# Kernel tuning notes

Hardware: AMD Instinct MI355X
Metric: run time of the kernel (lower is better)

## Reference

```python
import jax, jax.numpy as jnp
import numpy as np

MAX_POINTS = 2048  # config['object_points']


def setup_inputs() -> dict:
    key = jax.random.key(0)
    k1, k2 = jax.random.split(key)
    B, N, C = 64, 131072, 4
    point_cloud = jax.random.normal(k1, (B, N, C), dtype=jnp.float32)
    logits = jax.random.normal(k2, (B, 2, N), dtype=jnp.float32)
    return {"point_cloud": point_cloud, "logits": logits}


def reference(point_cloud, logits):
    """JAX translation of point_cloud_masking.

    point_cloud: (B, N, C) with xyz in channels 0:3
    logits:      (B, 2, N)
    Returns (object_point_cloud (B, M, 3), mask_xyz_mean (B, 3)).
    """
    M = MAX_POINTS
    B, N, _ = point_cloud.shape
    dtype = point_cloud.dtype

    mask = logits[:, 0, :] < logits[:, 1, :]                  # (B, N) bool
    maskf = mask.astype(dtype)
    count_f = jnp.sum(maskf, axis=1)                          # (B,)
    xyz = point_cloud[..., :3]                                # (B, N, 3)
    mask_xyz_mean = jnp.sum(maskf[..., None] * xyz, axis=1) / jnp.maximum(count_f, 1.0)[:, None]  # (B,3)
    centered = xyz - mask_xyz_mean[:, None, :]                # (B, N, 3)

    # Stable argsort puts masked-point indices first, preserving order (like torch.where).
    order = jnp.argsort(1 - maskf, axis=1, stable=True)       # (B, N) int
    cnt = count_f.astype(jnp.int32)                           # (B,)

    # Resample to fixed M points (with replacement), matching torch.randint semantics:
    #   cnt >  M: all M indices random in [0, cnt)
    #   cnt <  M: first cnt identity, remaining random in [0, cnt)
    #   cnt == M: identity
    ksel = jax.random.key(42)
    rand = jax.random.randint(ksel, (B, M), 0, jnp.maximum(cnt, 1)[:, None])
    j = jnp.arange(M, dtype=jnp.int32)[None, :]               # (1, M)
    keep = (j < cnt[:, None]) & (cnt[:, None] <= M)
    sel = jnp.where(keep, j, rand)                            # (B, M) positions into sorted order
    idx = jnp.take_along_axis(order, sel, axis=1)             # (B, M) original point indices
    obj = jnp.take_along_axis(centered, idx[..., None], axis=1)  # (B, M, 3)

    # Empty-mask fallback: ones * batch_index (matches torch branch).
    empty = (cnt == 0)[:, None, None]
    batch_ids = jnp.arange(B, dtype=dtype)[:, None, None]
    obj = jnp.where(empty, jnp.ones_like(obj) * batch_ids, obj)
    return obj, mask_xyz_mean
```

## Files before the change

### kernel.cpp

```cpp
#include <hip/hip_runtime.h>
#include <stdint.h>

#define BATCH 64
#define NPTS  131072
#define MPTS  2048
#define WORDS_PB (NPTS / 64)
#define P1_PPB 4096
#define P1_BLOCKS (BATCH * NPTS / P1_PPB)

struct U2 { uint32_t a, b; };

__host__ __device__ constexpr U2 tf2x32(uint32_t k0, uint32_t k1, uint32_t x0, uint32_t x1) {
  uint32_t ks0 = k0, ks1 = k1, ks2 = k0 ^ k1 ^ 0x1BD11BDAu;
  x0 += ks0; x1 += ks1;
  const int rotA[4] = {13, 15, 26, 6};
  const int rotB[4] = {17, 29, 16, 24};
  for (int r = 0; r < 4; ++r) { x0 += x1; x1 = (x1 << rotA[r]) | (x1 >> (32 - rotA[r])); x1 ^= x0; }
  x0 += ks1; x1 += ks2 + 1u;
  for (int r = 0; r < 4; ++r) { x0 += x1; x1 = (x1 << rotB[r]) | (x1 >> (32 - rotB[r])); x1 ^= x0; }
  x0 += ks2; x1 += ks0 + 2u;
  for (int r = 0; r < 4; ++r) { x0 += x1; x1 = (x1 << rotA[r]) | (x1 >> (32 - rotA[r])); x1 ^= x0; }
  x0 += ks0; x1 += ks1 + 3u;
  for (int r = 0; r < 4; ++r) { x0 += x1; x1 = (x1 << rotB[r]) | (x1 >> (32 - rotB[r])); x1 ^= x0; }
  x0 += ks1; x1 += ks2 + 4u;
  for (int r = 0; r < 4; ++r) { x0 += x1; x1 = (x1 << rotA[r]) | (x1 >> (32 - rotA[r])); x1 ^= x0; }
  x0 += ks2; x1 += ks0 + 5u;
  return U2{x0, x1};
}

__global__ __launch_bounds__(256) void pass1_kernel(
    const float4* __restrict__ pc, const float* __restrict__ lg,
    float* __restrict__ sums, unsigned long long* __restrict__ maskWords) {
  int blk = blockIdx.x;
  int t = threadIdx.x;
  size_t pbase = (size_t)blk * P1_PPB;
  int b = (int)(pbase >> 17);
  const float* l0g = lg + (size_t)b * NPTS;
  const float* l1g = lg + (size_t)(b + 1) * NPTS;

  float sx = 0.f, sy = 0.f, sz = 0.f;
#pragma unroll 2
  for (int half = 0; half < 2; ++half) {
#pragma unroll
    for (int k = 0; k < 8; ++k) {
      size_t p = pbase + (size_t)(half * 8 + k) * 256 + t;
      float a0 = l0g[p];
      float a1 = l1g[p];
      float4 q = pc[p];
      bool m = a0 < a1;
      unsigned long long bal = __ballot(m);
      if ((t & 63) == 0) maskWords[p >> 6] = bal;
      if (m) { sx += q.x; sy += q.y; sz += q.z; }
    }
  }

  for (int o = 32; o; o >>= 1) {
    sx += __shfl_down(sx, o, 64);
    sy += __shfl_down(sy, o, 64);
    sz += __shfl_down(sz, o, 64);
  }
  __shared__ float ssx[4], ssy[4], ssz[4];
  int wave = t >> 6;
  if ((t & 63) == 0) { ssx[wave] = sx; ssy[wave] = sy; ssz[wave] = sz; }
  __syncthreads();
  if (t == 0) {
    atomicAdd(&sums[b * 3 + 0], ssx[0] + ssx[1] + ssx[2] + ssx[3]);
    atomicAdd(&sums[b * 3 + 1], ssy[0] + ssy[1] + ssy[2] + ssy[3]);
    atomicAdd(&sums[b * 3 + 2], ssz[0] + ssz[1] + ssz[2] + ssz[3]);
  }
}

__global__ __launch_bounds__(256) void pass2_kernel(
    const unsigned long long* __restrict__ maskWords, const float* __restrict__ sums,
    uint32_t* __restrict__ wordOff, int* __restrict__ cnt,
    float* __restrict__ mean, float* __restrict__ out) {
  int b = blockIdx.x, t = threadIdx.x;
  int lane = t & 63, wv = t >> 6;
  const unsigned long long* mw = maskWords + (size_t)b * WORDS_PB;
  int base = t * 8;
  int p[8];
  int local = 0;
#pragma unroll
  for (int k = 0; k < 8; ++k) { p[k] = __popcll(mw[base + k]); local += p[k]; }

  int x = local;
#pragma unroll
  for (int o = 1; o < 64; o <<= 1) {
    int y = __shfl_up(x, o, 64);
    if (lane >= o) x += y;
  }
  __shared__ int wsum[4];
  if (lane == 63) wsum[wv] = x;
  __syncthreads();
  int add = 0;
#pragma unroll
  for (int u = 0; u < 4; ++u) add += (u < wv) ? wsum[u] : 0;
  int run = add + x - local;
  uint32_t* wo = wordOff + (size_t)b * WORDS_PB;
#pragma unroll
  for (int k = 0; k < 8; ++k) { wo[base + k] = (uint32_t)run; run += p[k]; }

  if (t == 0) {
    int ct = wsum[0] + wsum[1] + wsum[2] + wsum[3];
    cnt[b] = ct;
    float d  = fmaxf((float)ct, 1.0f);
    float mx = sums[b * 3 + 0] / d;
    float my = sums[b * 3 + 1] / d;
    float mz = sums[b * 3 + 2] / d;
    mean[b * 3 + 0] = mx; mean[b * 3 + 1] = my; mean[b * 3 + 2] = mz;
    float* om = out + (size_t)BATCH * MPTS * 3 + (size_t)b * 3;
    om[0] = mx; om[1] = my; om[2] = mz;
  }
}

__global__ __launch_bounds__(256) void pass3_kernel(
    const float4* __restrict__ pc, const int* __restrict__ cnt,
    const float* __restrict__ mean, const uint32_t* __restrict__ wordOff,
    const unsigned long long* __restrict__ maskWords,
    float* __restrict__ out) {
  int blk = blockIdx.x;
  int b = blk >> 3;
  int t = threadIdx.x;
  int j = (blk & 7) * 256 + t;
  int gid = b * MPTS + j;

  __shared__ uint32_t sOff[WORDS_PB];
  __shared__ float sMean[3];
  __shared__ int sCnt;
  const uint32_t* wo = wordOff + (size_t)b * WORDS_PB;
#pragma unroll
  for (int k = 0; k < 8; ++k) sOff[t + k * 256] = wo[t + k * 256];
  if (t < 3)  sMean[t] = mean[b * 3 + t];
  if (t == 0) sCnt = cnt[b];
  __syncthreads();

  int cb = sCnt;
  float ox, oy, oz;
  if (cb == 0) {
    ox = oy = oz = (float)b;
  } else {
    constexpr U2 K1 = tf2x32(0u, 42u, 0u, 0u);
    constexpr U2 K2 = tf2x32(0u, 42u, 0u, 1u);
    uint32_t span = (uint32_t)cb;
    U2 h = tf2x32(K1.a, K1.b, 0u, (uint32_t)gid);
    U2 l = tf2x32(K2.a, K2.b, 0u, (uint32_t)gid);
    uint32_t hb = h.a ^ h.b;
    uint32_t lb = l.a ^ l.b;
    uint32_t mul = 65536u % span;
    mul = (mul * mul) % span;
    uint32_t off = ((hb % span) * mul + (lb % span)) % span;
    int r = (j < cb && cb <= MPTS) ? j : (int)off;

    int lo = 0;
#pragma unroll
    for (int step = 1024; step; step >>= 1) {
      int nxt = lo + step;
      if (nxt < WORDS_PB && sOff[nxt] <= (uint32_t)r) lo = nxt;
    }
    int rem = r - (int)sOff[lo];
    unsigned long long w = maskWords[(size_t)b * WORDS_PB + lo];

    uint32_t cur = (uint32_t)w;
    int bitbase = 0;
    int c = __popc(cur);
    if (rem >= c) { rem -= c; cur = (uint32_t)(w >> 32); bitbase = 32; }
    c = __popc(cur & 0xFFFFu); if (rem >= c) { rem -= c; cur >>= 16; bitbase += 16; }
    c = __popc(cur & 0xFFu);   if (rem >= c) { rem -= c; cur >>= 8;  bitbase += 8;  }
    c = __popc(cur & 0xFu);    if (rem >= c) { rem -= c; cur >>= 4;  bitbase += 4;  }
    c = __popc(cur & 0x3u);    if (rem >= c) { rem -= c; cur >>= 2;  bitbase += 2;  }
    c = (int)(cur & 1u);       if (rem >= c) {           cur >>= 1;  bitbase += 1;  }
    int idx = lo * 64 + bitbase;

    float4 p = pc[(size_t)b * NPTS + idx];
    ox = p.x - sMean[0]; oy = p.y - sMean[1]; oz = p.z - sMean[2];
  }
  float* o = out + (size_t)gid * 3;
  o[0] = ox; o[1] = oy; o[2] = oz;
}

extern "C" void kernel_launch(void* const* d_in, const int* in_sizes, int n_in,
                              void* d_out, int out_size, void* d_ws, size_t ws_size,
                              hipStream_t stream) {
  const float4* pc = (const float4*)d_in[0];
  const float*  lg = (const float*)d_in[1];
  float* out = (float*)d_out;

  char* w = (char*)d_ws;
  float*    sums    = (float*)(w + 0);
  int*      cnt     = (int*)(w + 1024);
  float*    mean    = (float*)(w + 2048);
  uint32_t* wordOff = (uint32_t*)(w + 4096);
  unsigned long long* maskWords =
      (unsigned long long*)(w + 4096 + 524288);

  hipMemsetAsync(sums, 0, 768, stream);

  pass1_kernel<<<P1_BLOCKS, 256, 0, stream>>>(pc, lg, sums, maskWords);
  pass2_kernel<<<BATCH, 256, 0, stream>>>(maskWords, sums, wordOff, cnt, mean, out);
  pass3_kernel<<<(BATCH * MPTS) / 256, 256, 0, stream>>>(pc, cnt, mean, wordOff, maskWords, out);
}
```

Baseline: 248.7 us.

## Stage pass1 inputs into LDS with async global_load_lds and halve block size

The mask/sum pass now bulk-copies each block's point-cloud and logit tiles straight into shared memory with 16-byte global_load_lds, waits at one barrier, then computes from LDS instead of issuing per-thread global loads. Points per block drop from 4096 to 2048 so the roughly 48KB of staged data fits, which doubles the block count and the number of atomic partial-sum adds. The intent is to get more bytes in flight with wide, fully coalesced transfers. The cost is heavy LDS use, which can cap occupancy, plus a full barrier before any compute starts.

```diff
diff --git a/kernel.cpp b/kernel.cpp
--- a/kernel.cpp
+++ b/kernel.cpp
@@ -5,7 +5,7 @@
 #define NPTS  131072
 #define MPTS  2048
 #define WORDS_PB (NPTS / 64)
-#define P1_PPB 4096
+#define P1_PPB 2048
 #define P1_BLOCKS (BATCH * NPTS / P1_PPB)
 
 struct U2 { uint32_t a, b; };
@@ -28,30 +28,53 @@
   return U2{x0, x1};
 }
 
+__device__ __forceinline__ void load_lds16(const void* g, void* l) {
+  __builtin_amdgcn_global_load_lds(
+      (const __attribute__((address_space(1))) void*)g,
+      (__attribute__((address_space(3))) void*)l, 16, 0, 0);
+}
+
 __global__ __launch_bounds__(256) void pass1_kernel(
     const float4* __restrict__ pc, const float* __restrict__ lg,
     float* __restrict__ sums, unsigned long long* __restrict__ maskWords) {
   int blk = blockIdx.x;
   int t = threadIdx.x;
-  size_t pbase = (size_t)blk * P1_PPB;
-  int b = (int)(pbase >> 17);
-  const float* l0g = lg + (size_t)b * NPTS;
-  const float* l1g = lg + (size_t)(b + 1) * NPTS;
+  int wv = t >> 6, lane = t & 63;
+  size_t blockBase = (size_t)blk * P1_PPB;
+  int b = (int)(blockBase >> 17);
+  size_t off = blockBase & (NPTS - 1);
+  const float4* pcg = pc + blockBase;
+  const float*  l0g = lg + (size_t)b * (2 * NPTS) + off;
+  const float*  l1g = l0g + NPTS;
+
+  __shared__ float4 sPC[P1_PPB];
+  __shared__ float  sL0[P1_PPB];
+  __shared__ float  sL1[P1_PPB];
+
+#pragma unroll
+  for (int k = 0; k < 8; ++k) {
+    int p = wv * 512 + k * 64;
+    load_lds16(pcg + p + lane, &sPC[p]);
+  }
+#pragma unroll
+  for (int k = 0; k < 2; ++k) {
+    int f = wv * 512 + k * 256;
+    load_lds16((const float4*)(l0g + f) + lane, &sL0[f]);
+    load_lds16((const float4*)(l1g + f) + lane, &sL1[f]);
+  }
+  __syncthreads();
 
   float sx = 0.f, sy = 0.f, sz = 0.f;
-#pragma unroll 2
-  for (int half = 0; half < 2; ++half) {
-#pragma unroll
-    for (int k = 0; k < 8; ++k) {
-      size_t p = pbase + (size_t)(half * 8 + k) * 256 + t;
-      float a0 = l0g[p];
-      float a1 = l1g[p];
-      float4 q = pc[p];
-      bool m = a0 < a1;
-      unsigned long long bal = __ballot(m);
-      if ((t & 63) == 0) maskWords[p >> 6] = bal;
-      if (m) { sx += q.x; sy += q.y; sz += q.z; }
-    }
+#pragma unroll
+  for (int k = 0; k < 8; ++k) {
+    int idx = k * 256 + t;
+    float a0 = sL0[idx];
+    float a1 = sL1[idx];
+    float4 q = sPC[idx];
+    bool m = a0 < a1;
+    unsigned long long bal = __ballot(m);
+    if (lane == 0) maskWords[(blockBase + idx) >> 6] = bal;
+    if (m) { sx += q.x; sy += q.y; sz += q.z; }
   }
 
   for (int o = 32; o; o >>= 1) {
@@ -60,8 +83,7 @@
     sz += __shfl_down(sz, o, 64);
   }
   __shared__ float ssx[4], ssy[4], ssz[4];
-  int wave = t >> 6;
-  if ((t & 63) == 0) { ssx[wave] = sx; ssy[wave] = sy; ssz[wave] = sz; }
+  if (lane == 0) { ssx[wv] = sx; ssy[wv] = sy; ssz[wv] = sz; }
   __syncthreads();
   if (t == 0) {
     atomicAdd(&sums[b * 3 + 0], ssx[0] + ssx[1] + ssx[2] + ssx[3]);
```

New measurement: 255.7 us. +2.8%, slower.
